# Kernel tuning notes

Hardware: AMD Instinct MI355X
Metric: run time of the kernel (lower is better)

The kernel has to match this reference:

```python
import jax, jax.numpy as jnp
import numpy as np

D_MODEL = 1024
H = 16
DK = D_MODEL // H
S = 4096


def setup_inputs() -> dict:
    key = jax.random.key(0)
    ks = jax.random.split(key, 11)
    scale = 1.0 / np.sqrt(D_MODEL)
    return {
        "Q": jax.random.normal(ks[0], (S, D_MODEL), jnp.float32),
        "K": jax.random.normal(ks[1], (S, D_MODEL), jnp.float32),
        "V": jax.random.normal(ks[2], (S, D_MODEL), jnp.float32),
        # per-head projection weights, stacked: [h, d_model, d_k]
        "Wq": jax.random.normal(ks[3], (H, D_MODEL, DK), jnp.float32) * scale,
        "bq": jax.random.normal(ks[4], (H, DK), jnp.float32) * 0.01,
        "Wk": jax.random.normal(ks[5], (H, D_MODEL, DK), jnp.float32) * scale,
        "bk": jax.random.normal(ks[6], (H, DK), jnp.float32) * 0.01,
        "Wv": jax.random.normal(ks[7], (H, D_MODEL, DK), jnp.float32) * scale,
        "bv": jax.random.normal(ks[8], (H, DK), jnp.float32) * 0.01,
        # output projection (torch Linear convention: y = x @ Wo.T + bo)
        "Wo": jax.random.normal(ks[9], (D_MODEL, D_MODEL), jnp.float32) * scale,
        "bo": jax.random.normal(ks[10], (D_MODEL,), jnp.float32) * 0.01,
    }


def reference(Q, K, V, Wq, bq, Wk, bk, Wv, bv, Wo, bo):
    # per-head projections, vectorized over heads: [h, S, d_k]
    q = jnp.einsum("sd,hdk->hsk", Q, Wq) + bq[:, None, :]
    k = jnp.einsum("sd,hdk->hsk", K, Wk) + bk[:, None, :]
    v = jnp.einsum("sd,hdk->hsk", V, Wv) + bv[:, None, :]
    # scaled dot-product attention (full [h, S, S] scores, as in the original)
    scores = jnp.einsum("hsk,htk->hst", q, k) / jnp.sqrt(jnp.float32(DK))
    attn = jax.nn.softmax(scores, axis=-1)
    o = jnp.einsum("hst,htk->hsk", attn, v)
    # concat heads along feature dim: [S, h*d_k]
    x = jnp.transpose(o, (1, 0, 2)).reshape(S, D_MODEL)
    return x @ Wo.T + bo
```

## Files before the change

kernel.cpp:

```cpp
#include <hip/hip_runtime.h>

typedef unsigned short u16;
typedef unsigned int u32;
using f32x4 = __attribute__((ext_vector_type(4))) float;
using f32x16 = __attribute__((ext_vector_type(16))) float;
using u32x4 = __attribute__((ext_vector_type(4))) u32;
using bf16x8 = __attribute__((ext_vector_type(8))) __bf16;

#define DEV __device__ __forceinline__

DEV u16 f2bf(float f) {
  u32 x = __builtin_bit_cast(u32, f);
  return (u16)((x + 0x7fffu + ((x >> 16) & 1u)) >> 16);
}

DEV f32x4 mfma16(bf16x8 a, bf16x8 b, f32x4 c) {
  return __builtin_amdgcn_mfma_f32_16x16x32_bf16(a, b, c, 0, 0, 0);
}
DEV f32x16 mfma32(bf16x8 a, bf16x8 b, f32x16 c) {
  return __builtin_amdgcn_mfma_f32_32x32x16_bf16(a, b, c, 0, 0, 0);
}

DEV float ex2(float x) {
#if __has_builtin(__builtin_amdgcn_exp2f)
  return __builtin_amdgcn_exp2f(x);
#else
  float r;
  asm("v_exp_f32 %0, %1" : "=v"(r) : "v"(x));
  return r;
#endif
}

DEV int swz(int row, int byteInRow) {
  return row * 128 + ((((byteInRow >> 4) ^ (row & 7)) << 4) | (byteInRow & 15));
}

DEV u32 pkbf(float lo, float hi) {
  union { u32 u; __bf16 h[2]; } x;
  x.h[0] = (__bf16)lo; x.h[1] = (__bf16)hi;
  return x.u;
}

DEV void gload16(const u16* g, u16* l) {
  __builtin_amdgcn_global_load_lds((const __attribute__((address_space(1))) void*)g,
                                   (__attribute__((address_space(3))) void*)l, 16, 0, 0);
}

__global__ __launch_bounds__(256) void prep_kernel(
    const float* __restrict__ Q, const float* __restrict__ K, const float* __restrict__ V,
    const float* __restrict__ Wo, const float* __restrict__ Wq, const float* __restrict__ Wk,
    const float* __restrict__ Wv, u16* __restrict__ Qb, u16* __restrict__ Kb,
    u16* __restrict__ Vb, u16* __restrict__ Wob, u16* __restrict__ Tq, u16* __restrict__ Tk,
    u16* __restrict__ Tv) {
  __shared__ u16 t[64][68];
  int y = blockIdx.y, tid = threadIdx.x;
  if (y < 4) {
    if (y == 3 && blockIdx.x >= 1024) return;
    const float* in = y == 0 ? Q : y == 1 ? K : y == 2 ? V : Wo;
    u16* out = y == 0 ? Qb : y == 1 ? Kb : y == 2 ? Vb : Wob;
    int i = blockIdx.x * 256 + tid;
    float4 v = ((const float4*)in)[i];
    ushort4 w;
    w.x = f2bf(v.x); w.y = f2bf(v.y); w.z = f2bf(v.z); w.w = f2bf(v.w);
    ((ushort4*)out)[i] = w;
    return;
  }
  if (blockIdx.x >= 768) return;
  int which = blockIdx.x >> 8, h = (blockIdx.x >> 4) & 15, d0 = (blockIdx.x & 15) * 64;
  const float* W = which == 0 ? Wq : (which == 1 ? Wk : Wv);
  u16* T = which == 0 ? Tq : (which == 1 ? Tk : Tv);
#pragma unroll
  for (int i = 0; i < 4; ++i) {
    int c = i * 256 + tid;
    int r = c >> 4, c4 = (c & 15) * 4;
    float4 v = *(const float4*)(W + h * 65536 + (d0 + r) * 64 + c4);
    t[r][c4] = f2bf(v.x); t[r][c4 + 1] = f2bf(v.y);
    t[r][c4 + 2] = f2bf(v.z); t[r][c4 + 3] = f2bf(v.w);
  }
  __syncthreads();
#pragma unroll
  for (int i = 0; i < 4; ++i) {
    int ch = i * 256 + tid;
    int cc = ch >> 4, d4 = (ch & 15) * 4;
    ushort4 w;
    w.x = t[d4][cc]; w.y = t[d4 + 1][cc]; w.z = t[d4 + 2][cc]; w.w = t[d4 + 3][cc];
    *(ushort4*)(T + (h * 64 + cc) * 1024 + d0 + d4) = w;
  }
}

__global__ __launch_bounds__(256, 3) void gemm_qkv(
    const u16* __restrict__ Qb, const u16* __restrict__ Kb, const u16* __restrict__ Vb,
    const u16* __restrict__ Tq, const u16* __restrict__ Tk, const u16* __restrict__ Tv,
    const float* __restrict__ bq, const float* __restrict__ bk, const float* __restrict__ bv,
    u16* __restrict__ qh, u16* __restrict__ kh, u16* __restrict__ vTh, float sc) {
  __shared__ alignas(16) u16 lA[128 * 64];
  __shared__ alignas(16) u16 lB[128 * 64];
  int z = blockIdx.z;
  const u16* A = z == 0 ? Qb : z == 1 ? Kb : Vb;
  const u16* B = z == 0 ? Tq : z == 1 ? Tk : Tv;
  const float* bias = z == 0 ? bq : z == 1 ? bk : bv;
  int bm = blockIdx.x, bn = blockIdx.y;
  const char* gA = (const char*)(A + bm * 131072);
  const char* gB = (const char*)(B + bn * 131072);
  int tid = threadIdx.x;
  int wid = tid >> 6, lane = tid & 63, g = lane >> 4, ln = lane & 15;
  int wr = wid >> 1, wc = wid & 1;
  const char* sA[4]; const char* sB[4];
  u16* dA[4]; u16* dB[4];
#pragma unroll
  for (int i = 0; i < 4; ++i) {
    int c = i * 256 + tid, row = c >> 3, cc = c & 7;
    int sw = (cc ^ (row & 7)) << 4;
    sA[i] = gA + row * 2048 + sw;
    sB[i] = gB + row * 2048 + sw;
    dA[i] = (u16*)((char*)lA + i * 4096 + wid * 1024);
    dB[i] = (u16*)((char*)lB + i * 4096 + wid * 1024);
  }
  f32x4 acc[4][4] = {};
  for (int k0 = 0; k0 < 1024; k0 += 64) {
#pragma unroll
    for (int i = 0; i < 4; ++i) {
      gload16((const u16*)(sA[i] + k0 * 2), dA[i]);
      gload16((const u16*)(sB[i] + k0 * 2), dB[i]);
    }
    __syncthreads();
#pragma unroll
    for (int ks = 0; ks < 2; ++ks) {
      bf16x8 af[4], bfr[4];
#pragma unroll
      for (int mt = 0; mt < 4; ++mt) {
        int row = wr * 64 + mt * 16 + ln;
        af[mt] = *(const bf16x8*)((const char*)lA + swz(row, ks * 64 + g * 16));
      }
#pragma unroll
      for (int nt = 0; nt < 4; ++nt) {
        int row = wc * 64 + nt * 16 + ln;
        bfr[nt] = *(const bf16x8*)((const char*)lB + swz(row, ks * 64 + g * 16));
      }
#pragma unroll
      for (int mt = 0; mt < 4; ++mt)
#pragma unroll
        for (int nt = 0; nt < 4; ++nt)
          acc[mt][nt] = mfma16(af[mt], bfr[nt], acc[mt][nt]);
    }
    __syncthreads();
  }
  float scale = z == 0 ? sc : 1.f;
  float bv_[4];
#pragma unroll
  for (int nt = 0; nt < 4; ++nt) bv_[nt] = bias[bn * 128 + wc * 64 + nt * 16 + ln];
  if (z < 2) {
    u16* out = z == 0 ? qh : kh;
#pragma unroll
    for (int mt = 0; mt < 4; ++mt)
      for (int nt = 0; nt < 4; ++nt)
        for (int r = 0; r < 4; ++r) {
          int s = bm * 128 + wr * 64 + mt * 16 + g * 4 + r;
          int j = bn * 128 + wc * 64 + nt * 16 + ln;
          out[(j >> 6) * 262144 + s * 64 + (j & 63)] = f2bf((acc[mt][nt][r] + bv_[nt]) * scale);
        }
  } else {
#pragma unroll
    for (int mt = 0; mt < 4; ++mt)
      for (int nt = 0; nt < 4; ++nt) {
        int sb = bm * 128 + wr * 64 + mt * 16 + g * 4;
        int j = bn * 128 + wc * 64 + nt * 16 + ln;
        ushort4 w;
        w.x = f2bf(acc[mt][nt][0] + bv_[nt]);
        w.y = f2bf(acc[mt][nt][1] + bv_[nt]);
        w.z = f2bf(acc[mt][nt][2] + bv_[nt]);
        w.w = f2bf(acc[mt][nt][3] + bv_[nt]);
        *(ushort4*)(vTh + j * 4096 + sb) = w;
      }
  }
}

__global__ __launch_bounds__(256) void gemm_out(const u16* __restrict__ A,
                                                const u16* __restrict__ B,
                                                const float* __restrict__ bias,
                                                float* __restrict__ out) {
  __shared__ alignas(16) u16 lA[64 * 64];
  __shared__ alignas(16) u16 lB[128 * 64];
  int tid = threadIdx.x;
  int wid = tid >> 6, lane = tid & 63, g = lane >> 4, ln = lane & 15;
  int wr = wid >> 1, wc = wid & 1;
  int bm = blockIdx.x, bn = blockIdx.y;
  const char* gA = (const char*)(A + bm * 65536);
  const char* gB = (const char*)(B + bn * 131072);
  const char* sA[2]; const char* sB[4];
  u16* dA[2]; u16* dB[4];
#pragma unroll
  for (int i = 0; i < 4; ++i) {
    int c = i * 256 + tid, row = c >> 3, cc = c & 7;
    int sw = (cc ^ (row & 7)) << 4;
    if (i < 2) {
      sA[i] = gA + row * 2048 + sw;
      dA[i] = (u16*)((char*)lA + i * 4096 + wid * 1024);
    }
    sB[i] = gB + row * 2048 + sw;
    dB[i] = (u16*)((char*)lB + i * 4096 + wid * 1024);
  }
  f32x4 acc[2][4] = {};
  for (int k0 = 0; k0 < 1024; k0 += 64) {
#pragma unroll
    for (int i = 0; i < 2; ++i) gload16((const u16*)(sA[i] + k0 * 2), dA[i]);
#pragma unroll
    for (int i = 0; i < 4; ++i) gload16((const u16*)(sB[i] + k0 * 2), dB[i]);
    __syncthreads();
#pragma unroll
    for (int ks = 0; ks < 2; ++ks) {
      bf16x8 af[2], bfr[4];
#pragma unroll
      for (int mt = 0; mt < 2; ++mt) {
        int row = wr * 32 + mt * 16 + ln;
        af[mt] = *(const bf16x8*)((const char*)lA + swz(row, ks * 64 + g * 16));
      }
#pragma unroll
      for (int nt = 0; nt < 4; ++nt) {
        int row = wc * 64 + nt * 16 + ln;
        bfr[nt] = *(const bf16x8*)((const char*)lB + swz(row, ks * 64 + g * 16));
      }
#pragma unroll
      for (int mt = 0; mt < 2; ++mt)
#pragma unroll
        for (int nt = 0; nt < 4; ++nt)
          acc[mt][nt] = mfma16(af[mt], bfr[nt], acc[mt][nt]);
    }
    __syncthreads();
  }
  float bv_[4];
#pragma unroll
  for (int nt = 0; nt < 4; ++nt) bv_[nt] = bias[bn * 128 + wc * 64 + nt * 16 + ln];
#pragma unroll
  for (int mt = 0; mt < 2; ++mt)
    for (int nt = 0; nt < 4; ++nt)
      for (int r = 0; r < 4; ++r) {
        int s = bm * 64 + wr * 32 + mt * 16 + g * 4 + r;
        int j = bn * 128 + wc * 64 + nt * 16 + ln;
        out[s * 1024 + j] = acc[mt][nt][r] + bv_[nt];
      }
}

__global__ __launch_bounds__(512, 4) void flash_attn2(const u16* __restrict__ qh,
                                                      const u16* __restrict__ kh,
                                                      const u16* __restrict__ vT,
                                                      u16* __restrict__ x) {
  __shared__ alignas(16) char smem[66048];
  u16* lK = (u16*)smem;
  u16* lV = (u16*)(smem + 32768);
  float* lbuf = (float*)(smem + 65536);
  float* mergeBuf = (float*)smem;

  int tid = threadIdx.x;
  int wid = tid >> 6, lane = tid & 63;
  int grp = wid >> 2, sw = wid & 3;
  int lq = lane & 31, hi = lane >> 5;
  int nb = (blockIdx.x & 7) * 64 + (blockIdx.x >> 3);
  int h = nb >> 5, qt = nb & 31;

  const u16* gK = kh + h * 262144 + grp * 131072;
  const u16* gV = vT + h * 262144 + grp * 2048;
  u16* lKg = lK + grp * 8192;
  u16* lVg = lV + grp * 8192;

  bf16x8 qf[4];
  {
    const u16* gQ = qh + h * 262144 + (qt * 128 + sw * 32 + lq) * 64 + hi * 8;
#pragma unroll
    for (int st = 0; st < 4; ++st) qf[st] = *(const bf16x8*)(gQ + st * 16);
  }
  f32x16 o0 = {}, o1 = {}, ol = {};
  u32x4 onesw;
  onesw[0] = onesw[1] = onesw[2] = onesw[3] = 0x3F803F80u;
  bf16x8 ones = __builtin_bit_cast(bf16x8, onesw);

  int r8 = lane >> 3, pc = lane & 7;
  int rowA = sw * 16 + r8, rowB = rowA + 8;
  const u16* pKA = gK + rowA * 64 + ((pc ^ (rowA & 7)) << 3);
  const u16* pKB = gK + rowB * 64 + ((pc ^ (rowB & 7)) << 3);
  const u16* pVA = gV + rowA * 4096 + ((pc ^ (rowA & 7)) << 3);
  const u16* pVB = gV + rowB * 4096 + ((pc ^ (rowB & 7)) << 3);
  u16* dKA = lKg + (sw * 16) * 64;
  u16* dKB = dKA + 512;
  u16* dVA = lVg + (sw * 16) * 64;
  u16* dVB = dVA + 512;

  gload16(pKA, dKA); gload16(pKB, dKB);
  gload16(pVA, dVA); gload16(pVB, dVB);
  pKA += 4096; pKB += 4096;
  pVA += 64; pVB += 64;

  const int NT = 32;
  for (int t = 0; t < NT; ++t) {
    asm volatile("s_waitcnt vmcnt(0)" ::: "memory");
    __builtin_amdgcn_s_barrier();
    __builtin_amdgcn_sched_barrier(0);
    int cur = t & 1;
    if (t + 1 < NT) {
      int nxt = (cur ^ 1) * 4096;
      gload16(pKA, dKA + nxt); gload16(pKB, dKB + nxt);
      gload16(pVA, dVA + nxt); gload16(pVB, dVB + nxt);
      pKA += 4096; pKB += 4096; pVA += 64; pVB += 64;
    }
    const u16* lKc = lKg + cur * 4096;
    const u16* lVc = lVg + cur * 4096;
    f32x16 s0 = {}, s1 = {};
    __builtin_amdgcn_s_setprio(1);
#pragma unroll
    for (int st = 0; st < 4; ++st) {
      bf16x8 k0 = *(const bf16x8*)((const char*)lKc + swz(lq, st * 32 + hi * 16));
      bf16x8 k1 = *(const bf16x8*)((const char*)lKc + swz(32 + lq, st * 32 + hi * 16));
      s0 = mfma32(k0, qf[st], s0);
      s1 = mfma32(k1, qf[st], s1);
    }
    __builtin_amdgcn_s_setprio(0);
#pragma unroll
    for (int r = 0; r < 16; ++r) {
      s0[r] = ex2(s0[r]);
      s1[r] = ex2(s1[r]);
    }
    bf16x8 pa[4];
#pragma unroll
    for (int n = 0; n < 2; ++n)
#pragma unroll
      for (int b2 = 0; b2 < 2; ++b2) {
        int b = b2 * 8;
        u32x4 wv;
        if (n == 0) {
          wv[0] = pkbf(s0[b + 0], s0[b + 1]); wv[1] = pkbf(s0[b + 2], s0[b + 3]);
          wv[2] = pkbf(s0[b + 4], s0[b + 5]); wv[3] = pkbf(s0[b + 6], s0[b + 7]);
        } else {
          wv[0] = pkbf(s1[b + 0], s1[b + 1]); wv[1] = pkbf(s1[b + 2], s1[b + 3]);
          wv[2] = pkbf(s1[b + 4], s1[b + 5]); wv[3] = pkbf(s1[b + 6], s1[b + 7]);
        }
        pa[n * 2 + b2] = __builtin_bit_cast(bf16x8, wv);
      }
    __builtin_amdgcn_s_setprio(1);
#pragma unroll
    for (int st = 0; st < 4; ++st) {
      uint2 a0 = *(const uint2*)((const char*)lVc + swz(lq, st * 32 + hi * 8));
      uint2 a1 = *(const uint2*)((const char*)lVc + swz(lq, st * 32 + 16 + hi * 8));
      uint2 b0 = *(const uint2*)((const char*)lVc + swz(32 + lq, st * 32 + hi * 8));
      uint2 b1 = *(const uint2*)((const char*)lVc + swz(32 + lq, st * 32 + 16 + hi * 8));
      u32x4 w0; w0[0] = a0.x; w0[1] = a0.y; w0[2] = a1.x; w0[3] = a1.y;
      u32x4 w1; w1[0] = b0.x; w1[1] = b0.y; w1[2] = b1.x; w1[3] = b1.y;
      o0 = mfma32(pa[st], __builtin_bit_cast(bf16x8, w0), o0);
      o1 = mfma32(pa[st], __builtin_bit_cast(bf16x8, w1), o1);
      ol = mfma32(pa[st], ones, ol);
    }
    __builtin_amdgcn_s_setprio(0);
  }

  __syncthreads();
  if (grp == 1) {
#pragma unroll
    for (int r = 0; r < 16; ++r) {
      int rq = (r & 3) + 8 * (r >> 2) + 4 * hi;
      float* mb = mergeBuf + (sw * 32 + rq) * 64;
      mb[lq] = o0[r];
      mb[32 + lq] = o1[r];
      if (lq == 0) lbuf[sw * 32 + rq] = ol[r];
    }
  }
  __syncthreads();
  if (grp == 0) {
#pragma unroll
    for (int r = 0; r < 16; ++r) {
      int rq = (r & 3) + 8 * (r >> 2) + 4 * hi;
      float inv = 1.f / (ol[r] + lbuf[sw * 32 + rq]);
      const float* mb = mergeBuf + (sw * 32 + rq) * 64;
      int srow = qt * 128 + sw * 32 + rq;
      u16* xr = x + srow * 1024 + h * 64;
      xr[lq] = f2bf((o0[r] + mb[lq]) * inv);
      xr[32 + lq] = f2bf((o1[r] + mb[32 + lq]) * inv);
    }
  }
}

extern "C" void kernel_launch(void* const* d_in, const int* in_sizes, int n_in,
                              void* d_out, int out_size, void* d_ws, size_t ws_size,
                              hipStream_t stream) {
  (void)in_sizes; (void)n_in; (void)out_size; (void)ws_size;
  const float* Q  = (const float*)d_in[0];
  const float* K  = (const float*)d_in[1];
  const float* V  = (const float*)d_in[2];
  const float* Wq = (const float*)d_in[3];
  const float* bq = (const float*)d_in[4];
  const float* Wk = (const float*)d_in[5];
  const float* bk = (const float*)d_in[6];
  const float* Wv = (const float*)d_in[7];
  const float* bv = (const float*)d_in[8];
  const float* Wo = (const float*)d_in[9];
  const float* bo = (const float*)d_in[10];

  char* ws = (char*)d_ws;
  u16* Qb  = (u16*)(ws + (0ull << 20));
  u16* Kb  = (u16*)(ws + (8ull << 20));
  u16* Vb  = (u16*)(ws + (16ull << 20));
  u16* Tq  = (u16*)(ws + (24ull << 20));
  u16* Tk  = (u16*)(ws + (26ull << 20));
  u16* Tv  = (u16*)(ws + (28ull << 20));
  u16* Wob = (u16*)(ws + (30ull << 20));
  u16* qh  = (u16*)(ws + (32ull << 20));
  u16* kh  = (u16*)(ws + (40ull << 20));
  u16* vTh = (u16*)(ws + (48ull << 20));
  u16* xb  = (u16*)(ws + (56ull << 20));

  const float SC = 0.125f * 1.44269504089f;

  prep_kernel<<<dim3(4096, 5), 256, 0, stream>>>(Q, K, V, Wo, Wq, Wk, Wv,
                                                 Qb, Kb, Vb, Wob, Tq, Tk, Tv);

  gemm_qkv<<<dim3(32, 8, 3), 256, 0, stream>>>(Qb, Kb, Vb, Tq, Tk, Tv, bq, bk, bv,
                                               qh, kh, vTh, SC);

  flash_attn2<<<512, 512, 0, stream>>>(qh, kh, vTh, xb);

  gemm_out<<<dim3(64, 8), 256, 0, stream>>>(xb, Wob, bo, (float*)d_out);
}
```

Measured before the change: 157.0 us.

## Fuse fp32-to-bf16 conversion of Q/K/V into QKV projection GEMM loads

The separate prep pass that converted Q, K and V to bf16 in workspace is removed. The QKV GEMM now reads fp32 activations directly, converts them in registers and writes swizzled bf16 into LDS, while B still uses async global-to-LDS loads. The grid becomes 1D with a remapped block order that groups M tiles sharing the same weight tile. This saves a full read/write round trip of 48MB fp32 plus bf16 intermediates, but each GEMM block now reads fp32 (twice the bytes) through registers synchronously, and the 8 N-blocks reread each A tile.

```diff
diff --git a/kernel.cpp b/kernel.cpp
--- a/kernel.cpp
+++ b/kernel.cpp
@@ -47,22 +47,18 @@
 }
 
 __global__ __launch_bounds__(256) void prep_kernel(
-    const float* __restrict__ Q, const float* __restrict__ K, const float* __restrict__ V,
-    const float* __restrict__ Wo, const float* __restrict__ Wq, const float* __restrict__ Wk,
-    const float* __restrict__ Wv, u16* __restrict__ Qb, u16* __restrict__ Kb,
-    u16* __restrict__ Vb, u16* __restrict__ Wob, u16* __restrict__ Tq, u16* __restrict__ Tk,
+    const float* __restrict__ Wo, const float* __restrict__ Wq,
+    const float* __restrict__ Wk, const float* __restrict__ Wv,
+    u16* __restrict__ Wob, u16* __restrict__ Tq, u16* __restrict__ Tk,
     u16* __restrict__ Tv) {
   __shared__ u16 t[64][68];
   int y = blockIdx.y, tid = threadIdx.x;
-  if (y < 4) {
-    if (y == 3 && blockIdx.x >= 1024) return;
-    const float* in = y == 0 ? Q : y == 1 ? K : y == 2 ? V : Wo;
-    u16* out = y == 0 ? Qb : y == 1 ? Kb : y == 2 ? Vb : Wob;
+  if (y == 0) {
     int i = blockIdx.x * 256 + tid;
-    float4 v = ((const float4*)in)[i];
+    float4 v = ((const float4*)Wo)[i];
     ushort4 w;
     w.x = f2bf(v.x); w.y = f2bf(v.y); w.z = f2bf(v.z); w.w = f2bf(v.w);
-    ((ushort4*)out)[i] = w;
+    ((ushort4*)Wob)[i] = w;
     return;
   }
   if (blockIdx.x >= 768) return;
@@ -89,39 +85,50 @@
 }
 
 __global__ __launch_bounds__(256, 3) void gemm_qkv(
-    const u16* __restrict__ Qb, const u16* __restrict__ Kb, const u16* __restrict__ Vb,
+    const float* __restrict__ Qf, const float* __restrict__ Kf, const float* __restrict__ Vf,
     const u16* __restrict__ Tq, const u16* __restrict__ Tk, const u16* __restrict__ Tv,
     const float* __restrict__ bq, const float* __restrict__ bk, const float* __restrict__ bv,
     u16* __restrict__ qh, u16* __restrict__ kh, u16* __restrict__ vTh, float sc) {
   __shared__ alignas(16) u16 lA[128 * 64];
   __shared__ alignas(16) u16 lB[128 * 64];
-  int z = blockIdx.z;
-  const u16* A = z == 0 ? Qb : z == 1 ? Kb : Vb;
+  int b = blockIdx.x;
+  int bn = (b >> 3) & 7;
+  int pm = (b & 7) + 8 * (b >> 6);
+  int bm = pm & 31, z = pm >> 5;
+  const float* Af = z == 0 ? Qf : z == 1 ? Kf : Vf;
   const u16* B = z == 0 ? Tq : z == 1 ? Tk : Tv;
   const float* bias = z == 0 ? bq : z == 1 ? bk : bv;
-  int bm = blockIdx.x, bn = blockIdx.y;
-  const char* gA = (const char*)(A + bm * 131072);
+  const float* gAf = Af + bm * 131072;
   const char* gB = (const char*)(B + bn * 131072);
   int tid = threadIdx.x;
   int wid = tid >> 6, lane = tid & 63, g = lane >> 4, ln = lane & 15;
   int wr = wid >> 1, wc = wid & 1;
-  const char* sA[4]; const char* sB[4];
-  u16* dA[4]; u16* dB[4];
+  const char* sB[4];
+  u16* dB[4];
+  const float* sAf[4];
+  char* dAsw[4];
 #pragma unroll
   for (int i = 0; i < 4; ++i) {
     int c = i * 256 + tid, row = c >> 3, cc = c & 7;
     int sw = (cc ^ (row & 7)) << 4;
-    sA[i] = gA + row * 2048 + sw;
     sB[i] = gB + row * 2048 + sw;
-    dA[i] = (u16*)((char*)lA + i * 4096 + wid * 1024);
     dB[i] = (u16*)((char*)lB + i * 4096 + wid * 1024);
+    sAf[i] = gAf + row * 1024 + cc * 8;
+    dAsw[i] = (char*)lA + swz(row, cc * 16);
   }
   f32x4 acc[4][4] = {};
   for (int k0 = 0; k0 < 1024; k0 += 64) {
 #pragma unroll
+    for (int i = 0; i < 4; ++i) gload16((const u16*)(sB[i] + k0 * 2), dB[i]);
+#pragma unroll
     for (int i = 0; i < 4; ++i) {
-      gload16((const u16*)(sA[i] + k0 * 2), dA[i]);
-      gload16((const u16*)(sB[i] + k0 * 2), dB[i]);
+      const float* src = sAf[i] + k0;
+      float4 f0 = *(const float4*)(src);
+      float4 f1 = *(const float4*)(src + 4);
+      u32x4 wv;
+      wv[0] = pkbf(f0.x, f0.y); wv[1] = pkbf(f0.z, f0.w);
+      wv[2] = pkbf(f1.x, f1.y); wv[3] = pkbf(f1.z, f1.w);
+      *(u32x4*)(dAsw[i]) = wv;
     }
     __syncthreads();
 #pragma unroll
@@ -394,9 +401,6 @@
   const float* bo = (const float*)d_in[10];
 
   char* ws = (char*)d_ws;
-  u16* Qb  = (u16*)(ws + (0ull << 20));
-  u16* Kb  = (u16*)(ws + (8ull << 20));
-  u16* Vb  = (u16*)(ws + (16ull << 20));
   u16* Tq  = (u16*)(ws + (24ull << 20));
   u16* Tk  = (u16*)(ws + (26ull << 20));
   u16* Tv  = (u16*)(ws + (28ull << 20));
@@ -408,11 +412,10 @@
 
   const float SC = 0.125f * 1.44269504089f;
 
-  prep_kernel<<<dim3(4096, 5), 256, 0, stream>>>(Q, K, V, Wo, Wq, Wk, Wv,
-                                                 Qb, Kb, Vb, Wob, Tq, Tk, Tv);
-
-  gemm_qkv<<<dim3(32, 8, 3), 256, 0, stream>>>(Qb, Kb, Vb, Tq, Tk, Tv, bq, bk, bv,
-                                               qh, kh, vTh, SC);
+  prep_kernel<<<dim3(1024, 2), 256, 0, stream>>>(Wo, Wq, Wk, Wv, Wob, Tq, Tk, Tv);
+
+  gemm_qkv<<<768, 256, 0, stream>>>(Q, K, V, Tq, Tk, Tv, bq, bk, bv,
+                                    qh, kh, vTh, SC);
 
   flash_attn2<<<512, 512, 0, stream>>>(qh, kh, vTh, xb);
 
```

After: 158.0 us. No clear change (+0.6%).
